# Performance work log

Hardware: AMD Instinct MI355X
Metric: run time of the kernel (lower is better)

Reference implementation:

```python
import jax, jax.numpy as jnp
import numpy as np

B, N, D, E, R, V = 8, 256, 64, 64, 32, 64
D_MIN, D_MAX = 0.0, 20.0


def _ln(x, g, b, eps=1e-5):
    m = jnp.mean(x, -1, keepdims=True)
    v = jnp.mean(jnp.square(x - m), -1, keepdims=True)
    return (x - m) * jax.lax.rsqrt(v + eps) * g + b


def setup_inputs() -> dict:
    key = jax.random.key(0)
    ks = jax.random.split(key, 12)
    w = lambda k, s: jax.random.normal(k, s, jnp.float32) * 0.02
    emb = w(ks[0], (V, D)).at[0].set(0.0)  # padding_idx=0 -> zero row
    return {
        "ligand_atom": jax.random.randint(ks[1], (B, N), 0, V),
        "ligand_pos": jax.random.normal(ks[2], (B, N, 3), jnp.float32),
        "edge_mask": jnp.ones((B, N, N), jnp.float32),
        "emb_table": emb,
        "ne_w": w(ks[3], (D, D)), "ne_b": jnp.zeros((D,), jnp.float32),
        "ne_g": jnp.ones((D,), jnp.float32), "ne_beta": jnp.zeros((D,), jnp.float32),
        "ee_w1": w(ks[4], (2 * D + R, E)), "ee_b1": jnp.zeros((E,), jnp.float32),
        "ee_w2": w(ks[5], (E, E)), "ee_b2": jnp.zeros((E,), jnp.float32),
        "ee_w3": w(ks[6], (E, E)), "ee_b3": jnp.zeros((E,), jnp.float32),
        "ee_g": jnp.ones((E,), jnp.float32), "ee_beta": jnp.zeros((E,), jnp.float32),
        "na_w1": w(ks[7], (D + E, D)), "na_b1": jnp.zeros((D,), jnp.float32),
        "na_w2": w(ks[8], (D, D)), "na_b2": jnp.zeros((D,), jnp.float32),
        "na_w3": w(ks[9], (D, D)), "na_b3": jnp.zeros((D,), jnp.float32),
        "na_g": jnp.ones((D,), jnp.float32), "na_beta": jnp.zeros((D,), jnp.float32),
    }


def reference(ligand_atom, ligand_pos, edge_mask, emb_table,
              ne_w, ne_b, ne_g, ne_beta,
              ee_w1, ee_b1, ee_w2, ee_b2, ee_w3, ee_b3, ee_g, ee_beta,
              na_w1, na_b1, na_w2, na_b2, na_w3, na_b3, na_g, na_beta):
    # node_embedder: Embedding -> ReLU -> Linear -> LayerNorm
    node = _ln(jax.nn.relu(emb_table[ligand_atom]) @ ne_w + ne_b, ne_g, ne_beta)  # [B,N,D]

    # pairwise distances, masked
    diff = ligand_pos[:, None, :, :] - ligand_pos[:, :, None, :]
    dist = jnp.sqrt(jnp.sum(diff * diff, -1) + 1e-10) * edge_mask  # [B,N,N]

    # RBF featurization
    mu = jnp.linspace(D_MIN, D_MAX, R)
    sigma = (D_MAX - D_MIN) / R
    rbf = jnp.exp(-jnp.square((dist[..., None] - mu) / sigma)) * edge_mask[..., None]  # [B,N,N,R]

    # edge_embedder: first Linear decomposed over [src | tar | rbf] slices (same math
    # as concat+Linear, avoids materializing the [B,N,N,2D+R] concat)
    Ws, Wt, Wr = ee_w1[:D], ee_w1[D:2 * D], ee_w1[2 * D:]
    # src[b,i,j]=node[b,j] (unsqueeze(1)), tar[b,i,j]=node[b,i] (unsqueeze(2))
    h = jax.nn.relu((node @ Ws)[:, None] + (node @ Wt)[:, :, None]
                    + jnp.einsum('bijr,re->bije', rbf, Wr) + ee_b1)
    h = jax.nn.relu(h @ ee_w2 + ee_b2)
    edge = _ln(h @ ee_w3 + ee_b3, ee_g, ee_beta)  # [B,N,N,E]

    # masked mean over dim=1, gated by (atom type clamped at 1)
    denom = jnp.sum(edge_mask[..., None], axis=1) + 1e-10  # [B,N,1]
    gate = jnp.minimum(ligand_atom, 1).astype(edge.dtype)[..., None]
    agg = jnp.sum(edge, axis=1) / denom * gate  # [B,N,E]

    x = jnp.concatenate([node, agg], -1)
    x = jax.nn.relu(x @ na_w1 + na_b1)
    x = jax.nn.relu(x @ na_w2 + na_b2)
    x = _ln(x @ na_w3 + na_b3, na_g, na_beta)
    return node + x, edge
```

## Files before the change

kernel.cpp:

```cpp
#include <hip/hip_runtime.h>
#include <math.h>

#define NB 8
#define NN 256
#define ND 64
#define NE 64
#define NR 32

typedef short short8 __attribute__((ext_vector_type(8)));
typedef float f32x4 __attribute__((ext_vector_type(4)));

__device__ __forceinline__ unsigned short f2bf(float f) {
    unsigned int u = __float_as_uint(f);
    u += 0x7fffu + ((u >> 16) & 1u);
    return (unsigned short)(u >> 16);
}

__device__ __forceinline__ float rl(float x, int lane) {
    return __uint_as_float(__builtin_amdgcn_readlane(__float_as_uint(x), lane));
}

__device__ __forceinline__ float wave_sum64(float v) {
#pragma unroll
    for (int m = 32; m >= 1; m >>= 1) v += __shfl_xor(v, m, 64);
    return v;
}

__global__ __launch_bounds__(256) void k_prep(
    const float* __restrict__ ee_w1, const float* __restrict__ ee_w2,
    const float* __restrict__ ee_w3,
    unsigned short* __restrict__ wr_t, unsigned short* __restrict__ w2t,
    unsigned short* __restrict__ w3t)
{
    const int t = threadIdx.x;
    for (int idx = t; idx < NE * NR; idx += 256) {
        int e = idx >> 5, r = idx & 31;
        wr_t[idx] = f2bf(ee_w1[(2 * ND + r) * NE + e]);
    }
    for (int idx = t; idx < NE * NE; idx += 256) {
        int n = idx >> 6, k = idx & 63;
        w2t[idx] = f2bf(ee_w2[k * NE + n]);
        w3t[idx] = f2bf(ee_w3[k * NE + n]);
    }
}

__global__ __launch_bounds__(256) void k1_node(
    const int* __restrict__ atom, const float* __restrict__ emb,
    const float* __restrict__ ne_w, const float* __restrict__ ne_b,
    const float* __restrict__ ne_g, const float* __restrict__ ne_beta,
    const float* __restrict__ ee_w1, const float* __restrict__ ee_b1,
    float* __restrict__ ws_node, float* __restrict__ ws_s, float* __restrict__ ws_t)
{
    const int wave = threadIdx.x >> 6;
    const int lane = threadIdx.x & 63;
    const int row  = blockIdx.x * 4 + wave;

    const int a = atom[row];
    float ev = fmaxf(emb[a * ND + lane], 0.f);

    float a0 = 0.f, a1 = 0.f, a2 = 0.f, a3 = 0.f;
#pragma unroll
    for (int k = 0; k < ND; k += 4) {
        a0 = fmaf(rl(ev, k + 0), ne_w[(k + 0) * ND + lane], a0);
        a1 = fmaf(rl(ev, k + 1), ne_w[(k + 1) * ND + lane], a1);
        a2 = fmaf(rl(ev, k + 2), ne_w[(k + 2) * ND + lane], a2);
        a3 = fmaf(rl(ev, k + 3), ne_w[(k + 3) * ND + lane], a3);
    }
    float pre = ne_b[lane] + ((a0 + a1) + (a2 + a3));

    float mean = wave_sum64(pre) * (1.f / 64.f);
    float dv = pre - mean;
    float var = wave_sum64(dv * dv) * (1.f / 64.f);
    float nv = dv * rsqrtf(var + 1e-5f) * ne_g[lane] + ne_beta[lane];
    ws_node[row * ND + lane] = nv;

    float s0 = 0.f, s1 = 0.f, t0 = 0.f, t1 = 0.f;
#pragma unroll
    for (int k = 0; k < ND; k += 2) {
        float n0 = rl(nv, k), n1 = rl(nv, k + 1);
        s0 = fmaf(n0, ee_w1[(k)     * NE + lane], s0);
        s1 = fmaf(n1, ee_w1[(k + 1) * NE + lane], s1);
        t0 = fmaf(n0, ee_w1[(ND + k)     * NE + lane], t0);
        t1 = fmaf(n1, ee_w1[(ND + k + 1) * NE + lane], t1);
    }
    ws_s[row * NE + lane] = ee_b1[lane] + s0 + s1;
    ws_t[row * NE + lane] = t0 + t1;
}

__global__ __launch_bounds__(256, 2) void k2_edge(
    const float* __restrict__ pos, const float* __restrict__ mask,
    const int* __restrict__ atom,
    const float* __restrict__ ws_s, const float* __restrict__ ws_t,
    const unsigned short* __restrict__ wr_t, const unsigned short* __restrict__ w2t,
    const unsigned short* __restrict__ w3t,
    const float* __restrict__ ee_b2, const float* __restrict__ ee_b3,
    const float* __restrict__ ee_g, const float* __restrict__ ee_beta,
    float* __restrict__ edge_out, float* __restrict__ ws_agg)
{
    __shared__ unsigned short hbuf[4][64 * 72];
    __shared__ float aggp[4][64];
    __shared__ float mp[4];

    const int bj = blockIdx.x;
    const int b = bj >> 8, j = bj & 255;
    const int wave = threadIdx.x >> 6, lane = threadIdx.x & 63;
    const int quad = lane >> 4, col = lane & 15;
    const int ibase = wave * 64;

    short8 wrf[4], w2f[4][2], w3f[4][2];
#pragma unroll
    for (int nt = 0; nt < 4; nt++)
        wrf[nt] = *(const short8*)(wr_t + (nt * 16 + col) * NR + quad * 8);
#pragma unroll
    for (int nt = 0; nt < 4; nt++)
#pragma unroll
        for (int kt = 0; kt < 2; kt++) {
            w2f[nt][kt] = *(const short8*)(w2t + (nt * 16 + col) * NE + kt * 32 + quad * 8);
            w3f[nt][kt] = *(const short8*)(w3t + (nt * 16 + col) * NE + kt * 32 + quad * 8);
        }

    float sj[4], b2v[4], b3v[4], gv[4], bev[4];
#pragma unroll
    for (int nt = 0; nt < 4; nt++) {
        const int e = nt * 16 + col;
        sj[nt]  = ws_s[bj * NE + e];
        b2v[nt] = ee_b2[e];
        b3v[nt] = ee_b3[e];
        gv[nt]  = ee_g[e];
        bev[nt] = ee_beta[e];
    }

    const float pjx = pos[bj * 3 + 0], pjy = pos[bj * 3 + 1], pjz = pos[bj * 3 + 2];

    float murv[8];
#pragma unroll
    for (int t = 0; t < 8; t++) murv[t] = 1.0322580645f * (float)(quad * 8 + t);

    short8 af[4];
    float mrow[4];
#pragma unroll
    for (int mt = 0; mt < 4; mt++) {
        const int i = ibase + mt * 16 + col;
        const int bi = b * NN + i;
        const float m = mask[bi * NN + j];
        const float dx = pjx - pos[bi * 3 + 0];
        const float dy = pjy - pos[bi * 3 + 1];
        const float dz = pjz - pos[bi * 3 + 2];
        const float dist = sqrtf(fmaf(dx, dx, fmaf(dy, dy, fmaf(dz, dz, 1e-10f)))) * m;
        mrow[mt] = m;
        short8 a;
#pragma unroll
        for (int t = 0; t < 8; t++) {
            const float u = fmaf(dist, 1.6f, -murv[t]);
            const float rv = exp2f(u * u * (-1.44269504f)) * m;
            a[t] = (short)f2bf(rv);
        }
        af[mt] = a;
    }

    unsigned short* h = hbuf[wave];

    f32x4 acc[4][4];
#pragma unroll
    for (int mt = 0; mt < 4; mt++)
#pragma unroll
        for (int nt = 0; nt < 4; nt++) {
            f32x4 z = {0.f, 0.f, 0.f, 0.f};
            acc[mt][nt] = __builtin_amdgcn_mfma_f32_16x16x32_bf16(af[mt], wrf[nt], z, 0, 0, 0);
        }

    {
        const float* tb = ws_t + (b * NN + ibase + quad * 4) * NE + col;
#pragma unroll
        for (int mt = 0; mt < 4; mt++)
#pragma unroll
            for (int nt = 0; nt < 4; nt++)
#pragma unroll
                for (int r = 0; r < 4; r++) {
                    const float tv = tb[(mt * 16 + r) * NE + nt * 16];
                    const float hv = fmaxf(acc[mt][nt][r] + sj[nt] + tv, 0.f);
                    h[(mt * 16 + quad * 4 + r) * 72 + nt * 16 + col] = f2bf(hv);
                }
    }

    short8 a2[4][2];
#pragma unroll
    for (int mt = 0; mt < 4; mt++)
#pragma unroll
        for (int kt = 0; kt < 2; kt++)
            a2[mt][kt] = *(const short8*)(h + (mt * 16 + col) * 72 + kt * 32 + quad * 8);

    f32x4 acc2[4][4];
#pragma unroll
    for (int mt = 0; mt < 4; mt++)
#pragma unroll
        for (int nt = 0; nt < 4; nt++) {
            f32x4 z = {0.f, 0.f, 0.f, 0.f};
            z = __builtin_amdgcn_mfma_f32_16x16x32_bf16(a2[mt][0], w2f[nt][0], z, 0, 0, 0);
            acc2[mt][nt] = __builtin_amdgcn_mfma_f32_16x16x32_bf16(a2[mt][1], w2f[nt][1], z, 0, 0, 0);
        }

#pragma unroll
    for (int mt = 0; mt < 4; mt++)
#pragma unroll
        for (int nt = 0; nt < 4; nt++)
#pragma unroll
            for (int r = 0; r < 4; r++) {
                const float hv = fmaxf(acc2[mt][nt][r] + b2v[nt], 0.f);
                h[(mt * 16 + quad * 4 + r) * 72 + nt * 16 + col] = f2bf(hv);
            }

    short8 a3[4][2];
#pragma unroll
    for (int mt = 0; mt < 4; mt++)
#pragma unroll
        for (int kt = 0; kt < 2; kt++)
            a3[mt][kt] = *(const short8*)(h + (mt * 16 + col) * 72 + kt * 32 + quad * 8);

    f32x4 acc3[4][4];
#pragma unroll
    for (int mt = 0; mt < 4; mt++)
#pragma unroll
        for (int nt = 0; nt < 4; nt++) {
            f32x4 z = {0.f, 0.f, 0.f, 0.f};
            z = __builtin_amdgcn_mfma_f32_16x16x32_bf16(a3[mt][0], w3f[nt][0], z, 0, 0, 0);
            acc3[mt][nt] = __builtin_amdgcn_mfma_f32_16x16x32_bf16(a3[mt][1], w3f[nt][1], z, 0, 0, 0);
        }

#pragma unroll
    for (int mt = 0; mt < 4; mt++)
#pragma unroll
        for (int nt = 0; nt < 4; nt++)
#pragma unroll
            for (int r = 0; r < 4; r++)
                acc3[mt][nt][r] += b3v[nt];

    float meanv[4][4], rsv[4][4];
#pragma unroll
    for (int mt = 0; mt < 4; mt++)
#pragma unroll
        for (int r = 0; r < 4; r++) {
            float s = 0.f, q = 0.f;
#pragma unroll
            for (int nt = 0; nt < 4; nt++) {
                const float x = acc3[mt][nt][r];
                s += x;
                q = fmaf(x, x, q);
            }
#pragma unroll
            for (int m = 1; m <= 8; m <<= 1) {
                s += __shfl_xor(s, m, 64);
                q += __shfl_xor(q, m, 64);
            }
            const float mean = s * (1.f / 64.f);
            const float var = q * (1.f / 64.f) - mean * mean;
            meanv[mt][r] = mean;
            rsv[mt][r] = rsqrtf(var + 1e-5f);
        }

    float ag[4] = {0.f, 0.f, 0.f, 0.f};
    float* eb = edge_out + ((size_t)(b * NN + ibase + quad * 4) * NN + j) * NE + col;
#pragma unroll
    for (int mt = 0; mt < 4; mt++)
#pragma unroll
        for (int nt = 0; nt < 4; nt++)
#pragma unroll
            for (int r = 0; r < 4; r++) {
                const float d = (acc3[mt][nt][r] - meanv[mt][r]) * rsv[mt][r];
                const float y = fmaf(d, gv[nt], bev[nt]);
                eb[(mt * 16 + r) * NN * NE + nt * 16] = y;
                ag[nt] += y;
            }

#pragma unroll
    for (int nt = 0; nt < 4; nt++) {
        ag[nt] += __shfl_xor(ag[nt], 16, 64);
        ag[nt] += __shfl_xor(ag[nt], 32, 64);
    }
    if (quad == 0) {
#pragma unroll
        for (int nt = 0; nt < 4; nt++) aggp[wave][nt * 16 + col] = ag[nt];
    }
    float msu = mrow[0] + mrow[1] + mrow[2] + mrow[3];
#pragma unroll
    for (int m = 1; m <= 8; m <<= 1) msu += __shfl_xor(msu, m, 64);
    if (lane == 0) mp[wave] = msu;

    __syncthreads();
    if (threadIdx.x < 64) {
        const int e = threadIdx.x;
        const float tot = aggp[0][e] + aggp[1][e] + aggp[2][e] + aggp[3][e];
        const float ms = mp[0] + mp[1] + mp[2] + mp[3];
        const float gate = (atom[bj] > 0) ? 1.f : 0.f;
        ws_agg[bj * NE + e] = tot / (ms + 1e-10f) * gate;
    }
}

__global__ __launch_bounds__(256) void k3_final(
    const float* __restrict__ ws_node, const float* __restrict__ ws_agg,
    const float* __restrict__ na_w1, const float* __restrict__ na_b1,
    const float* __restrict__ na_w2, const float* __restrict__ na_b2,
    const float* __restrict__ na_w3, const float* __restrict__ na_b3,
    const float* __restrict__ na_g, const float* __restrict__ na_beta,
    float* __restrict__ out0)
{
    const int wave = threadIdx.x >> 6;
    const int lane = threadIdx.x & 63;
    const int row = blockIdx.x * 4 + wave;

    const float nv = ws_node[row * ND + lane];
    const float av = ws_agg[row * ND + lane];

    float a0 = 0.f, a1 = 0.f, a2 = 0.f, a3 = 0.f;
#pragma unroll
    for (int k = 0; k < ND; k += 2) {
        a0 = fmaf(rl(nv, k),     na_w1[(k)     * ND + lane], a0);
        a1 = fmaf(rl(nv, k + 1), na_w1[(k + 1) * ND + lane], a1);
        a2 = fmaf(rl(av, k),     na_w1[(ND + k)     * ND + lane], a2);
        a3 = fmaf(rl(av, k + 1), na_w1[(ND + k + 1) * ND + lane], a3);
    }
    const float x1 = fmaxf(na_b1[lane] + (a0 + a1) + (a2 + a3), 0.f);

    float b0 = 0.f, b1 = 0.f, b2 = 0.f, b3 = 0.f;
#pragma unroll
    for (int k = 0; k < ND; k += 4) {
        b0 = fmaf(rl(x1, k + 0), na_w2[(k + 0) * ND + lane], b0);
        b1 = fmaf(rl(x1, k + 1), na_w2[(k + 1) * ND + lane], b1);
        b2 = fmaf(rl(x1, k + 2), na_w2[(k + 2) * ND + lane], b2);
        b3 = fmaf(rl(x1, k + 3), na_w2[(k + 3) * ND + lane], b3);
    }
    const float x2 = fmaxf(na_b2[lane] + (b0 + b1) + (b2 + b3), 0.f);

    float c0 = 0.f, c1 = 0.f, c2 = 0.f, c3 = 0.f;
#pragma unroll
    for (int k = 0; k < ND; k += 4) {
        c0 = fmaf(rl(x2, k + 0), na_w3[(k + 0) * ND + lane], c0);
        c1 = fmaf(rl(x2, k + 1), na_w3[(k + 1) * ND + lane], c1);
        c2 = fmaf(rl(x2, k + 2), na_w3[(k + 2) * ND + lane], c2);
        c3 = fmaf(rl(x2, k + 3), na_w3[(k + 3) * ND + lane], c3);
    }
    const float p3 = na_b3[lane] + (c0 + c1) + (c2 + c3);

    const float mean = wave_sum64(p3) * (1.f / 64.f);
    const float dvv = p3 - mean;
    const float var = wave_sum64(dvv * dvv) * (1.f / 64.f);
    const float x3 = dvv * rsqrtf(var + 1e-5f) * na_g[lane] + na_beta[lane];

    out0[row * ND + lane] = nv + x3;
}

extern "C" void kernel_launch(void* const* d_in, const int* in_sizes, int n_in,
                              void* d_out, int out_size, void* d_ws, size_t ws_size,
                              hipStream_t stream) {
    const int*   atom    = (const int*)d_in[0];
    const float* pos     = (const float*)d_in[1];
    const float* mask    = (const float*)d_in[2];
    const float* emb     = (const float*)d_in[3];
    const float* ne_w    = (const float*)d_in[4];
    const float* ne_b    = (const float*)d_in[5];
    const float* ne_g    = (const float*)d_in[6];
    const float* ne_beta = (const float*)d_in[7];
    const float* ee_w1   = (const float*)d_in[8];
    const float* ee_b1   = (const float*)d_in[9];
    const float* ee_w2   = (const float*)d_in[10];
    const float* ee_b2   = (const float*)d_in[11];
    const float* ee_w3   = (const float*)d_in[12];
    const float* ee_b3   = (const float*)d_in[13];
    const float* ee_g    = (const float*)d_in[14];
    const float* ee_beta = (const float*)d_in[15];
    const float* na_w1   = (const float*)d_in[16];
    const float* na_b1   = (const float*)d_in[17];
    const float* na_w2   = (const float*)d_in[18];
    const float* na_b2   = (const float*)d_in[19];
    const float* na_w3   = (const float*)d_in[20];
    const float* na_b3   = (const float*)d_in[21];
    const float* na_g    = (const float*)d_in[22];
    const float* na_beta = (const float*)d_in[23];

    float* out0     = (float*)d_out;
    float* edge_out = (float*)d_out + NB * NN * ND;

    float* ws_node = (float*)d_ws;
    float* ws_s    = ws_node + NB * NN * ND;
    float* ws_t    = ws_s + NB * NN * NE;
    float* ws_agg  = ws_t + NB * NN * NE;
    unsigned short* wr_t = (unsigned short*)(ws_agg + NB * NN * NE);
    unsigned short* w2t  = wr_t + NE * NR;
    unsigned short* w3t  = w2t + NE * NE;

    hipLaunchKernelGGL(k_prep, dim3(1), dim3(256), 0, stream,
                       ee_w1, ee_w2, ee_w3, wr_t, w2t, w3t);

    hipLaunchKernelGGL(k1_node, dim3(NB * NN / 4), dim3(256), 0, stream,
                       atom, emb, ne_w, ne_b, ne_g, ne_beta, ee_w1, ee_b1,
                       ws_node, ws_s, ws_t);

    hipLaunchKernelGGL(k2_edge, dim3(NB * NN), dim3(256), 0, stream,
                       pos, mask, atom, ws_s, ws_t, wr_t, w2t, w3t,
                       ee_b2, ee_b3, ee_g, ee_beta, edge_out, ws_agg);

    hipLaunchKernelGGL(k3_final, dim3(NB * NN / 4), dim3(256), 0, stream,
                       ws_node, ws_agg, na_w1, na_b1, na_w2, na_b2, na_w3, na_b3,
                       na_g, na_beta, out0);
}
```

Before: 248.5 us.

## Chain edge MLP in registers via transposed fp16 MFMAs, fold target term into GEMM

The edge MLP now computes transposed products (features x edges), so each MFMA accumulator can be repacked directly into the next layer's B operand. This removes the LDS round-trips and their writes and reads between layers. The per-target node term is folded into the first GEMM by concatenating node features with the RBF inputs (K=96), so the ws_t buffer and its strided loads go away. Weights are switched from bf16 to fp16 and prepared inside the node kernel via extra blocks, which removes one launch. The cost is weights read from global or cache per k-step instead of held in registers, and fp16 range and precision differ from bf16.

New measurement: 249.1 us. About the same (+0.2%).

```diff
diff --git a/kernel.cpp b/kernel.cpp
--- a/kernel.cpp
+++ b/kernel.cpp
@@ -7,14 +7,10 @@
 #define NE 64
 #define NR 32
 
-typedef short short8 __attribute__((ext_vector_type(8)));
+typedef _Float16 half8 __attribute__((ext_vector_type(8)));
+typedef _Float16 half4 __attribute__((ext_vector_type(4)));
+typedef __fp16 fp16x2 __attribute__((ext_vector_type(2)));
 typedef float f32x4 __attribute__((ext_vector_type(4)));
-
-__device__ __forceinline__ unsigned short f2bf(float f) {
-    unsigned int u = __float_as_uint(f);
-    u += 0x7fffu + ((u >> 16) & 1u);
-    return (unsigned short)(u >> 16);
-}
 
 __device__ __forceinline__ float rl(float x, int lane) {
     return __uint_as_float(__builtin_amdgcn_readlane(__float_as_uint(x), lane));
@@ -26,22 +22,13 @@
     return v;
 }
 
-__global__ __launch_bounds__(256) void k_prep(
-    const float* __restrict__ ee_w1, const float* __restrict__ ee_w2,
-    const float* __restrict__ ee_w3,
-    unsigned short* __restrict__ wr_t, unsigned short* __restrict__ w2t,
-    unsigned short* __restrict__ w3t)
-{
-    const int t = threadIdx.x;
-    for (int idx = t; idx < NE * NR; idx += 256) {
-        int e = idx >> 5, r = idx & 31;
-        wr_t[idx] = f2bf(ee_w1[(2 * ND + r) * NE + e]);
-    }
-    for (int idx = t; idx < NE * NE; idx += 256) {
-        int n = idx >> 6, k = idx & 63;
-        w2t[idx] = f2bf(ee_w2[k * NE + n]);
-        w3t[idx] = f2bf(ee_w3[k * NE + n]);
-    }
+__device__ __forceinline__ half4 mk4(float a, float b, float c, float d) {
+    fp16x2 lo = __builtin_amdgcn_cvt_pkrtz(a, b);
+    fp16x2 hi = __builtin_amdgcn_cvt_pkrtz(c, d);
+    half4 r;
+    r[0] = (_Float16)lo[0]; r[1] = (_Float16)lo[1];
+    r[2] = (_Float16)hi[0]; r[3] = (_Float16)hi[1];
+    return r;
 }
 
 __global__ __launch_bounds__(256) void k1_node(
@@ -49,8 +36,27 @@
     const float* __restrict__ ne_w, const float* __restrict__ ne_b,
     const float* __restrict__ ne_g, const float* __restrict__ ne_beta,
     const float* __restrict__ ee_w1, const float* __restrict__ ee_b1,
-    float* __restrict__ ws_node, float* __restrict__ ws_s, float* __restrict__ ws_t)
+    const float* __restrict__ ee_w2, const float* __restrict__ ee_w3,
+    float* __restrict__ ws_node, float* __restrict__ ws_s,
+    _Float16* __restrict__ node_h, _Float16* __restrict__ wcat,
+    _Float16* __restrict__ w2tH, _Float16* __restrict__ w3tH)
 {
+    if (blockIdx.x >= 512) {
+        const int tid = (blockIdx.x - 512) * 256 + threadIdx.x;
+        for (int idx = tid; idx < 64 * 96; idx += 1024) {
+            const int e = idx / 96, k = idx - e * 96;
+            const float v = (k < 32) ? ee_w1[(2 * ND + k) * NE + e]
+                                     : ee_w1[(ND + (k - 32)) * NE + e];
+            wcat[idx] = (_Float16)v;
+        }
+        for (int idx = tid; idx < NE * NE; idx += 1024) {
+            const int n = idx >> 6, k = idx & 63;
+            w2tH[idx] = (_Float16)ee_w2[k * NE + n];
+            w3tH[idx] = (_Float16)ee_w3[k * NE + n];
+        }
+        return;
+    }
+
     const int wave = threadIdx.x >> 6;
     const int lane = threadIdx.x & 63;
     const int row  = blockIdx.x * 4 + wave;
@@ -73,31 +79,27 @@
     float var = wave_sum64(dv * dv) * (1.f / 64.f);
     float nv = dv * rsqrtf(var + 1e-5f) * ne_g[lane] + ne_beta[lane];
     ws_node[row * ND + lane] = nv;
-
-    float s0 = 0.f, s1 = 0.f, t0 = 0.f, t1 = 0.f;
+    node_h[row * ND + lane] = (_Float16)nv;
+
+    float s0 = 0.f, s1 = 0.f;
 #pragma unroll
     for (int k = 0; k < ND; k += 2) {
-        float n0 = rl(nv, k), n1 = rl(nv, k + 1);
-        s0 = fmaf(n0, ee_w1[(k)     * NE + lane], s0);
-        s1 = fmaf(n1, ee_w1[(k + 1) * NE + lane], s1);
-        t0 = fmaf(n0, ee_w1[(ND + k)     * NE + lane], t0);
-        t1 = fmaf(n1, ee_w1[(ND + k + 1) * NE + lane], t1);
+        s0 = fmaf(rl(nv, k),     ee_w1[(k)     * NE + lane], s0);
+        s1 = fmaf(rl(nv, k + 1), ee_w1[(k + 1) * NE + lane], s1);
     }
     ws_s[row * NE + lane] = ee_b1[lane] + s0 + s1;
-    ws_t[row * NE + lane] = t0 + t1;
-}
-
-__global__ __launch_bounds__(256, 2) void k2_edge(
+}
+
+__global__ __launch_bounds__(256) void k2_edge(
     const float* __restrict__ pos, const float* __restrict__ mask,
     const int* __restrict__ atom,
-    const float* __restrict__ ws_s, const float* __restrict__ ws_t,
-    const unsigned short* __restrict__ wr_t, const unsigned short* __restrict__ w2t,
-    const unsigned short* __restrict__ w3t,
+    const float* __restrict__ ws_s, const _Float16* __restrict__ node_h,
+    const _Float16* __restrict__ wcat, const _Float16* __restrict__ w2tH,
+    const _Float16* __restrict__ w3tH,
     const float* __restrict__ ee_b2, const float* __restrict__ ee_b3,
     const float* __restrict__ ee_g, const float* __restrict__ ee_beta,
     float* __restrict__ edge_out, float* __restrict__ ws_agg)
 {
-    __shared__ unsigned short hbuf[4][64 * 72];
     __shared__ float aggp[4][64];
     __shared__ float mp[4];
 
@@ -107,24 +109,19 @@
     const int quad = lane >> 4, col = lane & 15;
     const int ibase = wave * 64;
 
-    short8 wrf[4], w2f[4][2], w3f[4][2];
-#pragma unroll
-    for (int nt = 0; nt < 4; nt++)
-        wrf[nt] = *(const short8*)(wr_t + (nt * 16 + col) * NR + quad * 8);
-#pragma unroll
-    for (int nt = 0; nt < 4; nt++)
-#pragma unroll
-        for (int kt = 0; kt < 2; kt++) {
-            w2f[nt][kt] = *(const short8*)(w2t + (nt * 16 + col) * NE + kt * 32 + quad * 8);
-            w3f[nt][kt] = *(const short8*)(w3t + (nt * 16 + col) * NE + kt * 32 + quad * 8);
+    float s_r[4][4], b2_r[4][4];
+#pragma unroll
+    for (int mt = 0; mt < 4; mt++)
+#pragma unroll
+        for (int r = 0; r < 4; r++) {
+            const int e = mt * 16 + quad * 4 + r;
+            s_r[mt][r]  = ws_s[bj * NE + e];
+            b2_r[mt][r] = ee_b2[e];
         }
-
-    float sj[4], b2v[4], b3v[4], gv[4], bev[4];
+    float b3v[4], gv[4], bev[4];
 #pragma unroll
     for (int nt = 0; nt < 4; nt++) {
         const int e = nt * 16 + col;
-        sj[nt]  = ws_s[bj * NE + e];
-        b2v[nt] = ee_b2[e];
         b3v[nt] = ee_b3[e];
         gv[nt]  = ee_g[e];
         bev[nt] = ee_beta[e];
@@ -132,100 +129,120 @@
 
     const float pjx = pos[bj * 3 + 0], pjy = pos[bj * 3 + 1], pjz = pos[bj * 3 + 2];
 
-    float murv[8];
-#pragma unroll
-    for (int t = 0; t < 8; t++) murv[t] = 1.0322580645f * (float)(quad * 8 + t);
-
-    short8 af[4];
-    float mrow[4];
-#pragma unroll
-    for (int mt = 0; mt < 4; mt++) {
-        const int i = ibase + mt * 16 + col;
-        const int bi = b * NN + i;
+    float dist4[4], m4[4];
+#pragma unroll
+    for (int nt = 0; nt < 4; nt++) {
+        const int bi = b * NN + ibase + nt * 16 + col;
         const float m = mask[bi * NN + j];
         const float dx = pjx - pos[bi * 3 + 0];
         const float dy = pjy - pos[bi * 3 + 1];
         const float dz = pjz - pos[bi * 3 + 2];
-        const float dist = sqrtf(fmaf(dx, dx, fmaf(dy, dy, fmaf(dz, dz, 1e-10f)))) * m;
-        mrow[mt] = m;
-        short8 a;
-#pragma unroll
-        for (int t = 0; t < 8; t++) {
-            const float u = fmaf(dist, 1.6f, -murv[t]);
-            const float rv = exp2f(u * u * (-1.44269504f)) * m;
-            a[t] = (short)f2bf(rv);
+        dist4[nt] = sqrtf(fmaf(dx, dx, fmaf(dy, dy, fmaf(dz, dz, 1e-10f)))) * m;
+        m4[nt] = m;
+    }
+
+    float murv[8];
+#pragma unroll
+    for (int t = 0; t < 8; t++) murv[t] = 1.0322580645f * (float)(quad * 8 + t);
+
+    f32x4 acc1[4][4];
+#pragma unroll
+    for (int mt = 0; mt < 4; mt++)
+#pragma unroll
+        for (int nt = 0; nt < 4; nt++) acc1[mt][nt] = (f32x4){0.f, 0.f, 0.f, 0.f};
+
+#pragma unroll
+    for (int kt = 0; kt < 3; kt++) {
+        half8 bf[4];
+        if (kt == 0) {
+#pragma unroll
+            for (int nt = 0; nt < 4; nt++) {
+                const float d = dist4[nt], m = m4[nt];
+                half8 v;
+#pragma unroll
+                for (int t = 0; t < 8; t += 2) {
+                    const float u0 = fmaf(d, 1.6f, -murv[t]);
+                    const float u1 = fmaf(d, 1.6f, -murv[t + 1]);
+                    const float r0 = exp2f(u0 * u0 * (-1.44269504f)) * m;
+                    const float r1 = exp2f(u1 * u1 * (-1.44269504f)) * m;
+                    fp16x2 p = __builtin_amdgcn_cvt_pkrtz(r0, r1);
+                    v[t] = (_Float16)p[0]; v[t + 1] = (_Float16)p[1];
+                }
+                bf[nt] = v;
+            }
+        } else {
+#pragma unroll
+            for (int nt = 0; nt < 4; nt++) {
+                const int i = ibase + nt * 16 + col;
+                bf[nt] = *(const half8*)(node_h + (b * NN + i) * ND + (kt - 1) * 32 + quad * 8);
+            }
         }
-        af[mt] = a;
-    }
-
-    unsigned short* h = hbuf[wave];
-
-    f32x4 acc[4][4];
-#pragma unroll
-    for (int mt = 0; mt < 4; mt++)
-#pragma unroll
-        for (int nt = 0; nt < 4; nt++) {
-            f32x4 z = {0.f, 0.f, 0.f, 0.f};
-            acc[mt][nt] = __builtin_amdgcn_mfma_f32_16x16x32_bf16(af[mt], wrf[nt], z, 0, 0, 0);
-        }
-
-    {
-        const float* tb = ws_t + (b * NN + ibase + quad * 4) * NE + col;
+        half8 af[4];
 #pragma unroll
         for (int mt = 0; mt < 4; mt++)
+            af[mt] = *(const half8*)(wcat + (mt * 16 + col) * 96 + kt * 32 + quad * 8);
+#pragma unroll
+        for (int mt = 0; mt < 4; mt++)
 #pragma unroll
             for (int nt = 0; nt < 4; nt++)
-#pragma unroll
-                for (int r = 0; r < 4; r++) {
-                    const float tv = tb[(mt * 16 + r) * NE + nt * 16];
-                    const float hv = fmaxf(acc[mt][nt][r] + sj[nt] + tv, 0.f);
-                    h[(mt * 16 + quad * 4 + r) * 72 + nt * 16 + col] = f2bf(hv);
-                }
-    }
-
-    short8 a2[4][2];
-#pragma unroll
-    for (int mt = 0; mt < 4; mt++)
-#pragma unroll
-        for (int kt = 0; kt < 2; kt++)
-            a2[mt][kt] = *(const short8*)(h + (mt * 16 + col) * 72 + kt * 32 + quad * 8);
+                acc1[mt][nt] = __builtin_amdgcn_mfma_f32_16x16x32_f16(af[mt], bf[nt], acc1[mt][nt], 0, 0, 0);
+    }
+
+    half4 b1f[4][4];
+#pragma unroll
+    for (int mt = 0; mt < 4; mt++)
+#pragma unroll
+        for (int nt = 0; nt < 4; nt++)
+            b1f[mt][nt] = mk4(fmaxf(acc1[mt][nt][0] + s_r[mt][0], 0.f),
+                              fmaxf(acc1[mt][nt][1] + s_r[mt][1], 0.f),
+                              fmaxf(acc1[mt][nt][2] + s_r[mt][2], 0.f),
+                              fmaxf(acc1[mt][nt][3] + s_r[mt][3], 0.f));
 
     f32x4 acc2[4][4];
 #pragma unroll
     for (int mt = 0; mt < 4; mt++)
 #pragma unroll
-        for (int nt = 0; nt < 4; nt++) {
-            f32x4 z = {0.f, 0.f, 0.f, 0.f};
-            z = __builtin_amdgcn_mfma_f32_16x16x32_bf16(a2[mt][0], w2f[nt][0], z, 0, 0, 0);
-            acc2[mt][nt] = __builtin_amdgcn_mfma_f32_16x16x32_bf16(a2[mt][1], w2f[nt][1], z, 0, 0, 0);
-        }
-
+        for (int nt = 0; nt < 4; nt++) acc2[mt][nt] = (f32x4){0.f, 0.f, 0.f, 0.f};
+#pragma unroll
+    for (int kt = 0; kt < 4; kt++) {
+        half4 a2[4];
+#pragma unroll
+        for (int mt = 0; mt < 4; mt++)
+            a2[mt] = *(const half4*)(w2tH + (mt * 16 + col) * NE + kt * 16 + quad * 4);
+#pragma unroll
+        for (int mt = 0; mt < 4; mt++)
+#pragma unroll
+            for (int nt = 0; nt < 4; nt++)
+                acc2[mt][nt] = __builtin_amdgcn_mfma_f32_16x16x16f16(a2[mt], b1f[kt][nt], acc2[mt][nt], 0, 0, 0);
+    }
+
+    half4 a3f[4][4];
 #pragma unroll
     for (int mt = 0; mt < 4; mt++)
 #pragma unroll
         for (int nt = 0; nt < 4; nt++)
-#pragma unroll
-            for (int r = 0; r < 4; r++) {
-                const float hv = fmaxf(acc2[mt][nt][r] + b2v[nt], 0.f);
-                h[(mt * 16 + quad * 4 + r) * 72 + nt * 16 + col] = f2bf(hv);
-            }
-
-    short8 a3[4][2];
-#pragma unroll
-    for (int mt = 0; mt < 4; mt++)
-#pragma unroll
-        for (int kt = 0; kt < 2; kt++)
-            a3[mt][kt] = *(const short8*)(h + (mt * 16 + col) * 72 + kt * 32 + quad * 8);
+            a3f[nt][mt] = mk4(fmaxf(acc2[mt][nt][0] + b2_r[mt][0], 0.f),
+                              fmaxf(acc2[mt][nt][1] + b2_r[mt][1], 0.f),
+                              fmaxf(acc2[mt][nt][2] + b2_r[mt][2], 0.f),
+                              fmaxf(acc2[mt][nt][3] + b2_r[mt][3], 0.f));
 
     f32x4 acc3[4][4];
 #pragma unroll
     for (int mt = 0; mt < 4; mt++)
 #pragma unroll
-        for (int nt = 0; nt < 4; nt++) {
-            f32x4 z = {0.f, 0.f, 0.f, 0.f};
-            z = __builtin_amdgcn_mfma_f32_16x16x32_bf16(a3[mt][0], w3f[nt][0], z, 0, 0, 0);
-            acc3[mt][nt] = __builtin_amdgcn_mfma_f32_16x16x32_bf16(a3[mt][1], w3f[nt][1], z, 0, 0, 0);
-        }
+        for (int nt = 0; nt < 4; nt++) acc3[mt][nt] = (f32x4){0.f, 0.f, 0.f, 0.f};
+#pragma unroll
+    for (int kt = 0; kt < 4; kt++) {
+        half4 b3f[4];
+#pragma unroll
+        for (int nt = 0; nt < 4; nt++)
+            b3f[nt] = *(const half4*)(w3tH + (nt * 16 + col) * NE + kt * 16 + quad * 4);
+#pragma unroll
+        for (int mi = 0; mi < 4; mi++)
+#pragma unroll
+            for (int nt = 0; nt < 4; nt++)
+                acc3[mi][nt] = __builtin_amdgcn_mfma_f32_16x16x16f16(a3f[mi][kt], b3f[nt], acc3[mi][nt], 0, 0, 0);
+    }
 
 #pragma unroll
     for (int mt = 0; mt < 4; mt++)
@@ -281,7 +298,7 @@
 #pragma unroll
         for (int nt = 0; nt < 4; nt++) aggp[wave][nt * 16 + col] = ag[nt];
     }
-    float msu = mrow[0] + mrow[1] + mrow[2] + mrow[3];
+    float msu = m4[0] + m4[1] + m4[2] + m4[3];
 #pragma unroll
     for (int m = 1; m <= 8; m <<= 1) msu += __shfl_xor(msu, m, 64);
     if (lane == 0) mp[wave] = msu;
@@ -382,21 +399,18 @@
 
     float* ws_node = (float*)d_ws;
     float* ws_s    = ws_node + NB * NN * ND;
-    float* ws_t    = ws_s + NB * NN * NE;
-    float* ws_agg  = ws_t + NB * NN * NE;
-    unsigned short* wr_t = (unsigned short*)(ws_agg + NB * NN * NE);
-    unsigned short* w2t  = wr_t + NE * NR;
-    unsigned short* w3t  = w2t + NE * NE;
-
-    hipLaunchKernelGGL(k_prep, dim3(1), dim3(256), 0, stream,
-                       ee_w1, ee_w2, ee_w3, wr_t, w2t, w3t);
-
-    hipLaunchKernelGGL(k1_node, dim3(NB * NN / 4), dim3(256), 0, stream,
+    float* ws_agg  = ws_s + NB * NN * NE;
+    _Float16* node_h = (_Float16*)(ws_agg + NB * NN * NE);
+    _Float16* wcat   = node_h + NB * NN * ND;
+    _Float16* w2tH   = wcat + 64 * 96;
+    _Float16* w3tH   = w2tH + NE * NE;
+
+    hipLaunchKernelGGL(k1_node, dim3(516), dim3(256), 0, stream,
                        atom, emb, ne_w, ne_b, ne_g, ne_beta, ee_w1, ee_b1,
-                       ws_node, ws_s, ws_t);
+                       ee_w2, ee_w3, ws_node, ws_s, node_h, wcat, w2tH, w3tH);
 
     hipLaunchKernelGGL(k2_edge, dim3(NB * NN), dim3(256), 0, stream,
-                       pos, mask, atom, ws_s, ws_t, wr_t, w2t, w3t,
+                       pos, mask, atom, ws_s, node_h, wcat, w2tH, w3tH,
                        ee_b2, ee_b3, ee_g, ee_beta, edge_out, ws_agg);
 
     hipLaunchKernelGGL(k3_final, dim3(NB * NN / 4), dim3(256), 0, stream,
```
